# Optimization experiments

Measured on AMD Instinct MI355X. Metric: run time of the kernel, lower is better.

Reference implementation:

```python
import jax, jax.numpy as jnp
import numpy as np

DILATIONS = (1, 3, 5)
NUM_HEADS = 2


def _conv(x, w, b, dil=1, pad=0):
    # x: [B,C,H,W], w: [O,I,kh,kw] (OIHW), 'same'-style padding = dilation for k=3
    y = jax.lax.conv_general_dilated(
        x, w, window_strides=(1, 1), padding=[(pad, pad), (pad, pad)],
        rhs_dilation=(dil, dil), dimension_numbers=('NCHW', 'OIHW', 'NCHW'))
    return y + b[None, :, None, None]


def setup_inputs() -> dict:
    key = jax.random.key(0)
    ks = jax.random.split(key, 4)
    B, Cin, H, W = 4, 256, 64, 64
    Cout = 256
    x = jax.random.normal(ks[0], (B, Cin, H, W), dtype=jnp.float32)
    # kaiming-uniform-like init scale
    q_w = jax.random.uniform(ks[1], (Cout, Cin, 3, 3), dtype=jnp.float32,
                             minval=-1.0, maxval=1.0) * np.sqrt(6.0 / (Cin * 9))
    k_w = jax.random.uniform(ks[2], (Cout, Cin, 1, 1), dtype=jnp.float32,
                             minval=-1.0, maxval=1.0) * np.sqrt(6.0 / Cin)
    v_w = jax.random.uniform(ks[3], (Cout, Cin, 1, 1), dtype=jnp.float32,
                             minval=-1.0, maxval=1.0) * np.sqrt(6.0 / Cin)
    q_b = jnp.zeros((Cout,), jnp.float32)
    k_b = jnp.zeros((Cout,), jnp.float32)
    v_b = jnp.zeros((Cout,), jnp.float32)
    return {"x": x, "q_w": q_w, "q_b": q_b, "k_w": k_w, "k_b": k_b,
            "v_w": v_w, "v_b": v_b}


def reference(x, q_w, q_b, k_w, k_b, v_w, v_b):
    B, C, H, W = x.shape
    Cout = q_w.shape[0]
    hd = Cout // NUM_HEADS  # head_dim
    # ds_conv2d: sum of SiLU(dilated conv) over dilations 1,3,5 (padding=dilation)
    q = sum(jax.nn.silu(_conv(x, q_w, q_b, dil=d, pad=d)) for d in DILATIONS)
    k = _conv(x, k_w, k_b)
    v = _conv(x, v_w, v_b)
    N = H * W
    # [B, heads, head_dim, N]
    q = q.reshape(B, NUM_HEADS, hd, N)
    k = k.reshape(B, NUM_HEADS, hd, N)
    v = v.reshape(B, NUM_HEADS, hd, N)
    # energy[b,h,n,m] = sum_d q[b,h,d,n] * k[b,h,d,m]
    energy = jnp.einsum('bhdn,bhdm->bhnm', q, k)
    attn = jax.nn.softmax(energy / jnp.sqrt(jnp.float32(hd)), axis=-1)
    # out[b,h,n,d] = sum_m attn[b,h,n,m] * v[b,h,d,m]; then back to [B,C,H,W]
    out = jnp.einsum('bhnm,bhdm->bhdn', attn, v)
    return out.reshape(B, Cout, H, W)
```

## Files before the change

kernel.cpp:

```cpp
#include <hip/hip_runtime.h>
#include <cstdint>

typedef __attribute__((ext_vector_type(8))) _Float16 f16x8;
typedef __attribute__((ext_vector_type(4))) float f32x4;

#define DEV static __device__ __forceinline__

DEV void gld_lds16(void* lds_base, const void* gsrc) {
  __builtin_amdgcn_global_load_lds(
      (const __attribute__((address_space(1))) unsigned int*)gsrc,
      (__attribute__((address_space(3))) unsigned int*)lds_base,
      16, 0, 0);
}
DEV unsigned short f2h(float f) {
  _Float16 h = (_Float16)f;
  return __builtin_bit_cast(unsigned short, h);
}
DEV float h2f(unsigned short u) {
  _Float16 h = __builtin_bit_cast(_Float16, u);
  return (float)h;
}
DEV unsigned pk2h(float a, float b) {
  auto h2 = __builtin_amdgcn_cvt_pkrtz(a, b);
  return __builtin_bit_cast(unsigned, h2);
}
DEV float v_exp2(float x) { float r; asm("v_exp_f32 %0, %1" : "=v"(r) : "v"(x)); return r; }
DEV float v_rcp(float x) { float r; asm("v_rcp_f32 %0, %1" : "=v"(r) : "v"(x)); return r; }


__global__ __launch_bounds__(256) void k_prep_x(const float* __restrict__ x, char* __restrict__ xpad) {
  __shared__ float xs[32 * 257];
  int h = blockIdx.x, b = blockIdx.y, t = threadIdx.x;
  const float* xb = x + (size_t)b * 1048576 + h * 64;
  for (int half = 0; half < 2; half++) {
    int w0 = half * 32;
    for (int kk = 0; kk < 32; kk++) {
      int flat = kk * 256 + t;
      int ci = flat >> 5, w = flat & 31;
      xs[w * 257 + ci] = xb[ci * 4096 + w0 + w];
    }
    __syncthreads();
    for (int g = 0; g < 4; g++) {
      int w = g * 8 + (t >> 5);
      int cg = t & 31;
      float v0 = xs[w * 257 + cg * 8 + 0], v1 = xs[w * 257 + cg * 8 + 1];
      float v2 = xs[w * 257 + cg * 8 + 2], v3 = xs[w * 257 + cg * 8 + 3];
      float v4 = xs[w * 257 + cg * 8 + 4], v5 = xs[w * 257 + cg * 8 + 5];
      float v6 = xs[w * 257 + cg * 8 + 6], v7 = xs[w * 257 + cg * 8 + 7];
      uint4 pk;
      pk.x = pk2h(v0, v1);
      pk.y = pk2h(v2, v3);
      pk.z = pk2h(v4, v5);
      pk.w = pk2h(v6, v7);
      *(uint4*)(xpad + ((size_t)((b * 74 + h + 5) * 74) + w0 + w + 5) * 512 + cg * 16) = pk;
    }
    __syncthreads();
  }
}

__global__ __launch_bounds__(256) void k_prep_w(
    const float* __restrict__ qw, const float* __restrict__ kw, const float* __restrict__ vw,
    unsigned short* __restrict__ Wq, unsigned short* __restrict__ Wk, unsigned short* __restrict__ Wv) {
  int gid = blockIdx.x * 256 + threadIdx.x;
  const float* q9 = qw + (size_t)gid * 9;
#pragma unroll
  for (int tp = 0; tp < 9; tp++) Wq[tp * 65536 + gid] = f2h(q9[tp]);
  Wk[gid] = f2h(kw[gid]);
  Wv[gid] = f2h(vw[gid]);
}

__global__ __launch_bounds__(256, 2) void k_conv_kv(
    const char* __restrict__ xpad, const unsigned short* __restrict__ Wk,
    const unsigned short* __restrict__ Wv, const float* __restrict__ kb,
    const float* __restrict__ vb, unsigned short* __restrict__ K, unsigned short* __restrict__ V) {
  __shared__ char sm[32768];
  char* Xs = sm;
  char* Ws = sm + 16384;
  int t = threadIdx.x, lane = t & 63, wid = t >> 6, q4 = lane >> 4, l15 = lane & 15;
  int px0 = blockIdx.x * 128;
  int b = px0 >> 12, nn = px0 & 4095;
  int h = blockIdx.y;
  int mode = blockIdx.z;
  int co0 = h * 128;
  const char* Wsrc = (const char*)(mode ? Wv : Wk);
  int wm = wid & 1, wn = wid >> 1;
  f32x4 acc[4][4] = {};
  for (int c = 0; c < 4; c++) {
    __syncthreads();
    for (int ch = wid * 1024; ch < 16384; ch += 4096) {
      int o = ch + lane * 16;
      int r = o >> 7;
      int n = nn + r, hh = n >> 6, ww2 = n & 63;
      int col = (o & 127) ^ ((r & 7) << 4);
      gld_lds16(Xs + ch, xpad + ((size_t)((b * 74 + hh + 5) * 74) + ww2 + 5) * 512 + c * 128 + col);
    }
    for (int ch = wid * 1024; ch < 16384; ch += 4096) {
      int o = ch + lane * 16;
      int r = o >> 7;
      int col = (o & 127) ^ ((r & 7) << 4);
      gld_lds16(Ws + ch, Wsrc + (co0 + r) * 512 + c * 128 + col);
    }
    asm volatile("s_waitcnt vmcnt(0)" ::: "memory");
    __syncthreads();
    int xg = mode ? wn : wm;
    int wg = mode ? wm : wn;
#pragma unroll
    for (int kt = 0; kt < 2; kt++) {
      f16x8 xf[4], wf[4];
#pragma unroll
      for (int i = 0; i < 4; i++) {
        int rx = xg * 64 + i * 16 + l15;
        xf[i] = *(const f16x8*)(Xs + ((rx * 128 + kt * 64 + q4 * 16) ^ ((rx & 7) << 4)));
        int rw = wg * 64 + i * 16 + l15;
        wf[i] = *(const f16x8*)(Ws + ((rw * 128 + kt * 64 + q4 * 16) ^ ((rw & 7) << 4)));
      }
#pragma unroll
      for (int m = 0; m < 4; m++)
#pragma unroll
        for (int n = 0; n < 4; n++)
          acc[m][n] = mode ? __builtin_amdgcn_mfma_f32_16x16x32_f16(wf[m], xf[n], acc[m][n], 0, 0, 0)
                           : __builtin_amdgcn_mfma_f32_16x16x32_f16(xf[m], wf[n], acc[m][n], 0, 0, 0);
    }
  }
  int bh = b * 2 + h;
  if (mode == 0) {
#pragma unroll
    for (int m = 0; m < 4; m++)
#pragma unroll
      for (int n = 0; n < 4; n++) {
        int dd = wn * 64 + n * 16 + l15;
        float bias = kb[co0 + dd];
#pragma unroll
        for (int j = 0; j < 4; j++) {
          int npix = nn + wm * 64 + m * 16 + q4 * 4 + j;
          K[(size_t)(bh * 4096 + npix) * 128 + dd] = f2h(acc[m][n][j] + bias);
        }
      }
  } else {
#pragma unroll
    for (int m = 0; m < 4; m++)
#pragma unroll
      for (int j = 0; j < 4; j++) {
        int cr = wm * 64 + m * 16 + q4 * 4 + j;
        float bias = vb[co0 + cr];
#pragma unroll
        for (int n = 0; n < 4; n++) {
          int pc = nn + wn * 64 + (n >> 1) * 32 + (l15 >> 2) * 8 + (n & 1) * 4 + (l15 & 3);
          V[(size_t)(bh * 128 + cr) * 4096 + pc] = f2h(acc[m][n][j] + bias);
        }
      }
  }
}

__global__ __launch_bounds__(256, 2) void k_conv_q(
    const char* __restrict__ xpad, const unsigned short* __restrict__ Wq,
    const float* __restrict__ qb, unsigned short* __restrict__ Q) {
  extern __shared__ char sm[];
  char* Bs = sm;
  char* As = sm + 49152;
  int t = threadIdx.x, lane = t & 63, wid = t >> 6, q4 = lane >> 4, l15 = lane & 15;
  int fblk = blockIdx.x;
  int g = (fblk & 7) * 64 + (fblk >> 3);
  int h = g & 63, b = (g >> 6) & 3, ch2 = g >> 8;
  int co0 = ch2 * 128;
  int wm = wid & 1, wn = wid >> 1;
  const int dil[3] = {1, 3, 5};
  f32x4 accd[3][2][4] = {};
  for (int kh = 0; kh < 3; kh++) {
    for (int c = 0; c < 4; c++) {
      __syncthreads();
      const char* wq_base = (const char*)Wq + kh * 3 * 131072 + co0 * 512 + c * 128;
      for (int ch = wid * 1024; ch < 49152; ch += 4096) {
        int o = ch + lane * 16;
        int kw = o >> 14;
        int r = (o >> 7) & 127;
        int col = (o & 127) ^ ((r & 7) << 4);
        gld_lds16(Bs + ch, wq_base + kw * 131072 + r * 512 + col);
      }
      int nst = (kh == 1) ? 1 : 3;
      for (int di = 0; di < nst; di++) {
        int pr = h + (kh - 1) * dil[di] + 5;
        const char* gsrc = xpad + (size_t)((b * 74 + pr) * 74) * 512 + c * 128;
        char* Ad = As + di * 10240;
        for (int ch = wid * 1024; ch < 9472; ch += 4096) {
          int o = ch + lane * 16;
          if (o < 9472) {
            int r = o >> 7;
            int col = (o & 127) ^ ((r & 7) << 4);
            gld_lds16(Ad + ch, gsrc + r * 512 + col);
          }
        }
      }
      asm volatile("s_waitcnt vmcnt(0)" ::: "memory");
      __syncthreads();
#pragma unroll
      for (int kw = 0; kw < 3; kw++) {
        f16x8 bf[4][2];
#pragma unroll
        for (int n = 0; n < 4; n++)
#pragma unroll
          for (int kt = 0; kt < 2; kt++) {
            int rc = wn * 64 + n * 16 + l15;
            bf[n][kt] = *(const f16x8*)(Bs + kw * 16384 + ((rc * 128 + kt * 64 + q4 * 16) ^ ((rc & 7) << 4)));
          }
#pragma unroll
        for (int di = 0; di < 3; di++) {
          int d = dil[di];
          const char* Ad = As + (kh == 1 ? 0 : di) * 10240;
          int dw = (kw - 1) * d + 5;
          f16x8 af[2][2];
#pragma unroll
          for (int m = 0; m < 2; m++)
#pragma unroll
            for (int kt = 0; kt < 2; kt++) {
              int wp = wm * 32 + m * 16 + l15 + dw;
              af[m][kt] = *(const f16x8*)(Ad + ((wp * 128 + kt * 64 + q4 * 16) ^ ((wp & 7) << 4)));
            }
#pragma unroll
          for (int m = 0; m < 2; m++)
#pragma unroll
            for (int n = 0; n < 4; n++)
#pragma unroll
              for (int kt = 0; kt < 2; kt++)
                accd[di][m][n] = __builtin_amdgcn_mfma_f32_16x16x32_f16(af[m][kt], bf[n][kt], accd[di][m][n], 0, 0, 0);
        }
      }
    }
  }
  const float LOG2E = 1.4426950408889634f;
  const float QSCALE = 0.12751879523176862f;
#pragma unroll
  for (int n = 0; n < 4; n++) {
    float bias = qb[co0 + wn * 64 + n * 16 + l15];
#pragma unroll
    for (int m = 0; m < 2; m++)
#pragma unroll
      for (int j = 0; j < 4; j++) {
        float s = 0.f;
#pragma unroll
        for (int di = 0; di < 3; di++) {
          float v = accd[di][m][n][j] + bias;
          s += v * v_rcp(1.0f + v_exp2(-v * LOG2E));
        }
        int px = wm * 32 + m * 16 + q4 * 4 + j;
        int dd = wn * 64 + n * 16 + l15;
        int npix = h * 64 + px;
        Q[((size_t)(b * 2 + ch2) * 4096 + npix) * 128 + dd] = f2h(s * QSCALE);
      }
  }
}

__global__ __launch_bounds__(256, 2) void k_attn(
    const unsigned short* __restrict__ Q, const unsigned short* __restrict__ K,
    const unsigned short* __restrict__ V, float* __restrict__ out,
    unsigned short* __restrict__ o1buf, float* __restrict__ mlbuf) {
  __shared__ char sm[65536];
  char* K0 = sm;
  char* K1 = sm + 16384;
  char* V0 = sm + 32768;
  char* V1 = sm + 49152;
  int t = threadIdx.x, lane = t & 63, wid = t >> 6, q4 = lane >> 4, l15 = lane & 15;
  int fblk = blockIdx.x;
  int g = (fblk & 7) * 64 + (fblk >> 3);
  int nb = g & 31, bh = (g >> 5) & 7, half = g >> 8;
  int b = bh >> 1, hh = bh & 1;
  int n0 = nb * 128;
  const char* Qg = (const char*)(Q + ((size_t)bh * 4096 + n0) * 128);
  const char* Kg = (const char*)(K + (size_t)bh * 4096 * 128) + half * 524288;
  const char* Vg = (const char*)(V + (size_t)bh * 128 * 4096) + half * 4096;
  f16x8 qf[2][4];
#pragma unroll
  for (int nt = 0; nt < 2; nt++)
#pragma unroll
    for (int kt = 0; kt < 4; kt++) {
      int rn = wid * 32 + nt * 16 + l15;
      qf[nt][kt] = *(const f16x8*)(Qg + (size_t)rn * 256 + kt * 64 + q4 * 16);
    }
  for (int ch = wid * 1024; ch < 16384; ch += 4096) {
    int o = ch + lane * 16;
    gld_lds16(K0 + ch, Kg + (o ^ (((o >> 8) & 15) << 4)));
  }
  for (int ch = wid * 1024; ch < 16384; ch += 4096) {
    int o = ch + lane * 16;
    int dd = o >> 7;
    int col = (o & 127) ^ ((dd & 7) << 4);
    gld_lds16(V0 + ch, Vg + dd * 8192 + col);
  }
  asm volatile("s_waitcnt vmcnt(0)" ::: "memory");
  __syncthreads();
  f32x4 Ofr[8][2] = {};
  float mrun[2] = {-3e38f, -3e38f};
  float lrun[2] = {0.f, 0.f};
  for (int it = 0; it < 32; it++) {
    char* Kc = (it & 1) ? K1 : K0;
    char* Vc = (it & 1) ? V1 : V0;
    if (it < 31) {
      char* Kn = (it & 1) ? K0 : K1;
      char* Vn = (it & 1) ? V0 : V1;
      const char* kg = Kg + (size_t)(it + 1) * 16384;
      for (int ch = wid * 1024; ch < 16384; ch += 4096) {
        int o = ch + lane * 16;
        gld_lds16(Kn + ch, kg + (o ^ (((o >> 8) & 15) << 4)));
      }
      const char* vg = Vg + (it + 1) * 128;
      for (int ch = wid * 1024; ch < 16384; ch += 4096) {
        int o = ch + lane * 16;
        int dd = o >> 7;
        int col = (o & 127) ^ ((dd & 7) << 4);
        gld_lds16(Vn + ch, vg + dd * 8192 + col);
      }
    }
    f32x4 sT[4][2] = {};
#pragma unroll
    for (int kt = 0; kt < 4; kt++) {
      f16x8 kf[4];
#pragma unroll
      for (int mt = 0; mt < 4; mt++) {
        int rm = mt * 16 + l15;
        kf[mt] = *(const f16x8*)(Kc + ((rm * 256 + kt * 64 + q4 * 16) ^ ((rm & 15) << 4)));
      }
      __builtin_amdgcn_s_setprio(1);
#pragma unroll
      for (int mt = 0; mt < 4; mt++)
#pragma unroll
        for (int nt = 0; nt < 2; nt++)
          sT[mt][nt] = __builtin_amdgcn_mfma_f32_16x16x32_f16(kf[mt], qf[nt][kt], sT[mt][nt], 0, 0, 0);
      __builtin_amdgcn_s_setprio(0);
    }
    unsigned U[2][4][2];
#pragma unroll
    for (int nt = 0; nt < 2; nt++) {
      float mx = sT[0][nt][0];
#pragma unroll
      for (int mt = 0; mt < 4; mt++)
#pragma unroll
        for (int j = 0; j < 4; j++) mx = fmaxf(mx, sT[mt][nt][j]);
      mx = fmaxf(mx, __shfl_xor(mx, 16));
      mx = fmaxf(mx, __shfl_xor(mx, 32));
      float mn = mrun[nt];
      if (!__all(mx - mn <= 8.f)) {
        mn = fmaxf(mrun[nt], mx);
        float al = v_exp2(mrun[nt] - mn);
        mrun[nt] = mn;
        lrun[nt] *= al;
#pragma unroll
        for (int dt = 0; dt < 8; dt++) Ofr[dt][nt] *= al;
      }
      float rs = 0.f;
#pragma unroll
      for (int mt = 0; mt < 4; mt++) {
        float p0 = v_exp2(sT[mt][nt][0] - mn);
        float p1 = v_exp2(sT[mt][nt][1] - mn);
        float p2 = v_exp2(sT[mt][nt][2] - mn);
        float p3 = v_exp2(sT[mt][nt][3] - mn);
        rs += (p0 + p1) + (p2 + p3);
        U[nt][mt][0] = pk2h(p0, p1);
        U[nt][mt][1] = pk2h(p2, p3);
      }
      rs += __shfl_xor(rs, 16);
      rs += __shfl_xor(rs, 32);
      lrun[nt] += rs;
    }
#pragma unroll
    for (int kt = 0; kt < 2; kt++) {
      f16x8 pf[2];
#pragma unroll
      for (int nt = 0; nt < 2; nt++) {
        uint4 fr;
        fr.x = U[nt][2 * kt][0];
        fr.y = U[nt][2 * kt][1];
        fr.z = U[nt][2 * kt + 1][0];
        fr.w = U[nt][2 * kt + 1][1];
        pf[nt] = __builtin_bit_cast(f16x8, fr);
      }
      f16x8 vf[8];
#pragma unroll
      for (int dt = 0; dt < 8; dt++) {
        int rd = dt * 16 + l15;
        vf[dt] = *(const f16x8*)(Vc + ((rd * 128 + kt * 64 + q4 * 16) ^ ((rd & 7) << 4)));
      }
      __builtin_amdgcn_s_setprio(1);
#pragma unroll
      for (int dt = 0; dt < 8; dt++)
#pragma unroll
        for (int nt = 0; nt < 2; nt++)
          Ofr[dt][nt] = __builtin_amdgcn_mfma_f32_16x16x32_f16(vf[dt], pf[nt], Ofr[dt][nt], 0, 0, 0);
      __builtin_amdgcn_s_setprio(0);
    }
    __syncthreads();
  }
  if (q4 == 0) {
#pragma unroll
    for (int nt = 0; nt < 2; nt++) {
      int n = n0 + wid * 32 + nt * 16 + l15;
      float2 ml;
      ml.x = mrun[nt];
      ml.y = lrun[nt];
      *(float2*)(mlbuf + ((size_t)(half * 8 + bh) * 4096 + n) * 2) = ml;
    }
  }
  if (half == 0) {
    float* og = out + (size_t)(b * 256 + hh * 128) * 4096 + n0 + wid * 32;
#pragma unroll
    for (int dt = 0; dt < 8; dt++)
#pragma unroll
      for (int nt = 0; nt < 2; nt++)
#pragma unroll
        for (int j = 0; j < 4; j++) {
          int dd = dt * 16 + q4 * 4 + j;
          og[(size_t)dd * 4096 + nt * 16 + l15] = Ofr[dt][nt][j];
        }
  } else {
    float li[2] = {v_rcp(lrun[0]), v_rcp(lrun[1])};
    unsigned short* og = o1buf + (size_t)bh * 128 * 4096 + n0 + wid * 32;
#pragma unroll
    for (int dt = 0; dt < 8; dt++)
#pragma unroll
      for (int nt = 0; nt < 2; nt++)
#pragma unroll
        for (int j = 0; j < 4; j++) {
          int dd = dt * 16 + q4 * 4 + j;
          og[(size_t)dd * 4096 + nt * 16 + l15] = f2h(Ofr[dt][nt][j] * li[nt]);
        }
  }
}

__global__ __launch_bounds__(256) void k_combine(
    float* __restrict__ out, const unsigned short* __restrict__ o1,
    const float* __restrict__ ml) {
  int tid = blockIdx.x * 256 + threadIdx.x;
  int n = tid & 4095, dg = (tid >> 12) & 7, bh = tid >> 15;
  float2 ml0 = *(const float2*)(ml + ((size_t)bh * 4096 + n) * 2);
  float2 ml1 = *(const float2*)(ml + ((size_t)(8 + bh) * 4096 + n) * 2);
  float ms = fmaxf(ml0.x, ml1.x);
  float a0 = v_exp2(ml0.x - ms);
  float w1 = ml1.y * v_exp2(ml1.x - ms);
  float inv = 1.f / (ml0.y * a0 + w1);
  size_t ob = ((size_t)((bh >> 1) * 256 + (bh & 1) * 128 + dg * 16)) * 4096 + n;
  size_t o1b = ((size_t)(bh * 128 + dg * 16)) * 4096 + n;
#pragma unroll 4
  for (int j = 0; j < 16; j++) {
    float v0 = out[ob + (size_t)j * 4096];
    float v1 = h2f(o1[o1b + (size_t)j * 4096]);
    out[ob + (size_t)j * 4096] = (v0 * a0 + v1 * w1) * inv;
  }
}

extern "C" void kernel_launch(void* const* d_in, const int* in_sizes, int n_in,
                              void* d_out, int out_size, void* d_ws, size_t ws_size,
                              hipStream_t stream) {
  (void)in_sizes; (void)n_in; (void)out_size;
  const float* x  = (const float*)d_in[0];
  const float* qw = (const float*)d_in[1];
  const float* qb = (const float*)d_in[2];
  const float* kw = (const float*)d_in[3];
  const float* kb = (const float*)d_in[4];
  const float* vw = (const float*)d_in[5];
  const float* vb = (const float*)d_in[6];
  char* ws = (char*)d_ws;
  if (ws_size < 37822464) return;
  char* xpad = ws;
  unsigned short* Wq = (unsigned short*)(ws + 11214848);
  unsigned short* Wk = (unsigned short*)(ws + 12394496);
  unsigned short* Wv = (unsigned short*)(ws + 12525568);
  unsigned short* Qb = (unsigned short*)(ws + 12656640);
  unsigned short* Kb = (unsigned short*)(ws + 21045248);
  unsigned short* Vb = (unsigned short*)(ws + 29433856);
  unsigned short* O1 = (unsigned short*)ws;
  float* ML = (float*)(ws + 11214848);
  hipMemsetAsync(xpad, 0, 11214848, stream);
  k_prep_x<<<dim3(64, 4), dim3(256), 0, stream>>>(x, xpad);
  k_prep_w<<<dim3(256), dim3(256), 0, stream>>>(qw, kw, vw, Wq, Wk, Wv);
  k_conv_kv<<<dim3(128, 2, 2), dim3(256), 0, stream>>>(xpad, Wk, Wv, kb, vb, Kb, Vb);
  k_conv_q<<<dim3(512), dim3(256), 79872, stream>>>(xpad, Wq, qb, Qb);
  k_attn<<<dim3(512), dim3(256), 0, stream>>>(Qb, Kb, Vb, (float*)d_out, O1, ML);
  k_combine<<<dim3(1024), dim3(256), 0, stream>>>((float*)d_out, O1, ML);
}
```

Measured before the change: 179.7 us.

## Restructure dilated Q conv: two rows per block, double-buffered weight staging

The Q convolution kernel now runs 512 threads per block, each block covering two output image rows, so every weight tile loaded into LDS is reused across twice as many pixels and the grid halves. Weight tiles are staged one kw slice at a time into a double buffer, with the next slice prefetched while MFMAs run on the current one. MFMA bursts are also wrapped in s_setprio. Costs include a larger LDS footprint (89.6KB), a barrier after every kw step, and input-row staging that still waits synchronously.

New measurement: 179.2 us. About the same (-0.2%).

```diff
diff --git a/kernel.cpp b/kernel.cpp
--- a/kernel.cpp
+++ b/kernel.cpp
@@ -152,70 +152,95 @@
   }
 }
 
-__global__ __launch_bounds__(256, 2) void k_conv_q(
+__global__ __launch_bounds__(512, 2) void k_conv_q(
     const char* __restrict__ xpad, const unsigned short* __restrict__ Wq,
     const float* __restrict__ qb, unsigned short* __restrict__ Q) {
   extern __shared__ char sm[];
-  char* Bs = sm;
-  char* As = sm + 49152;
+  char* As = sm + 32768;
   int t = threadIdx.x, lane = t & 63, wid = t >> 6, q4 = lane >> 4, l15 = lane & 15;
   int fblk = blockIdx.x;
-  int g = (fblk & 7) * 64 + (fblk >> 3);
-  int h = g & 63, b = (g >> 6) & 3, ch2 = g >> 8;
+  int g = (fblk & 7) * 32 + (fblk >> 3);
+  int h2 = g & 31, b = (g >> 5) & 3, ch2 = g >> 7;
+  int h0 = h2 * 2;
   int co0 = ch2 * 128;
-  int wm = wid & 1, wn = wid >> 1;
+  int wn = wid & 1, wq = wid >> 1;
+  int hr = wq >> 1, wloc = wq & 1;
   const int dil[3] = {1, 3, 5};
+  const char* WqB = (const char*)Wq;
   f32x4 accd[3][2][4] = {};
+
+#define STAGE_B(dstbuf, kh_, c_, kw_)                                             \
+  {                                                                               \
+    const char* src_ = WqB + (size_t)((kh_)*3 + (kw_)) * 131072 + co0 * 512 + (c_)*128; \
+    char* dst_ = (dstbuf);                                                        \
+    for (int ch = wid * 1024; ch < 16384; ch += 8192) {                           \
+      int o = ch + lane * 16;                                                     \
+      int r = o >> 7;                                                             \
+      int col = (o & 127) ^ ((r & 7) << 4);                                       \
+      gld_lds16(dst_ + ch, src_ + r * 512 + col);                                 \
+    }                                                                             \
+  }
+
+#define STAGE_A_ROW(slot_, pr_, c_)                                               \
+  {                                                                               \
+    const char* src_ = xpad + ((size_t)(b * 74 + (pr_)) * 74) * 512 + (c_)*128;   \
+    char* dst_ = As + (slot_)*9472;                                               \
+    for (int ch = wid * 1024; ch < 9472; ch += 8192) {                            \
+      int o = ch + lane * 16;                                                     \
+      if (o < 9472) {                                                             \
+        int r = o >> 7;                                                           \
+        int col = (o & 127) ^ ((r & 7) << 4);                                     \
+        gld_lds16(dst_ + ch, src_ + r * 512 + col);                               \
+      }                                                                           \
+    }                                                                             \
+  }
+
+#define STAGE_A(kh_, c_)                                                          \
+  {                                                                               \
+    if ((kh_) == 1) {                                                             \
+      for (int s = 0; s < 2; s++) STAGE_A_ROW(s, h0 + s + 5, c_);                 \
+    } else {                                                                      \
+      for (int di = 0; di < 3; di++)                                              \
+        for (int s = 0; s < 2; s++)                                               \
+          STAGE_A_ROW(di * 2 + s, h0 + s + ((kh_)-1) * dil[di] + 5, c_);          \
+    }                                                                             \
+  }
+
+  STAGE_A(0, 0);
+  STAGE_B(sm, 0, 0, 0);
+  asm volatile("s_waitcnt vmcnt(0)" ::: "memory");
+  __syncthreads();
+
+  int cur = 0;
   for (int kh = 0; kh < 3; kh++) {
     for (int c = 0; c < 4; c++) {
-      __syncthreads();
-      const char* wq_base = (const char*)Wq + kh * 3 * 131072 + co0 * 512 + c * 128;
-      for (int ch = wid * 1024; ch < 49152; ch += 4096) {
-        int o = ch + lane * 16;
-        int kw = o >> 14;
-        int r = (o >> 7) & 127;
-        int col = (o & 127) ^ ((r & 7) << 4);
-        gld_lds16(Bs + ch, wq_base + kw * 131072 + r * 512 + col);
-      }
-      int nst = (kh == 1) ? 1 : 3;
-      for (int di = 0; di < nst; di++) {
-        int pr = h + (kh - 1) * dil[di] + 5;
-        const char* gsrc = xpad + (size_t)((b * 74 + pr) * 74) * 512 + c * 128;
-        char* Ad = As + di * 10240;
-        for (int ch = wid * 1024; ch < 9472; ch += 4096) {
-          int o = ch + lane * 16;
-          if (o < 9472) {
-            int r = o >> 7;
-            int col = (o & 127) ^ ((r & 7) << 4);
-            gld_lds16(Ad + ch, gsrc + r * 512 + col);
-          }
-        }
-      }
-      asm volatile("s_waitcnt vmcnt(0)" ::: "memory");
-      __syncthreads();
-#pragma unroll
       for (int kw = 0; kw < 3; kw++) {
+        int kwn = kw + 1, cn = c, khn = kh;
+        if (kwn == 3) { kwn = 0; cn = c + 1; if (cn == 4) { cn = 0; khn = kh + 1; } }
+        char* Bnext = cur ? sm : sm + 16384;
+        if (khn < 3) STAGE_B(Bnext, khn, cn, kwn);
+        const char* Bc = cur ? sm + 16384 : sm;
         f16x8 bf[4][2];
 #pragma unroll
         for (int n = 0; n < 4; n++)
 #pragma unroll
           for (int kt = 0; kt < 2; kt++) {
             int rc = wn * 64 + n * 16 + l15;
-            bf[n][kt] = *(const f16x8*)(Bs + kw * 16384 + ((rc * 128 + kt * 64 + q4 * 16) ^ ((rc & 7) << 4)));
+            bf[n][kt] = *(const f16x8*)(Bc + ((rc * 128 + kt * 64 + q4 * 16) ^ ((rc & 7) << 4)));
           }
 #pragma unroll
         for (int di = 0; di < 3; di++) {
-          int d = dil[di];
-          const char* Ad = As + (kh == 1 ? 0 : di) * 10240;
-          int dw = (kw - 1) * d + 5;
+          int dw = (kw - 1) * dil[di] + 5;
+          const char* Ad = As + (kh == 1 ? hr : di * 2 + hr) * 9472;
           f16x8 af[2][2];
 #pragma unroll
           for (int m = 0; m < 2; m++)
 #pragma unroll
             for (int kt = 0; kt < 2; kt++) {
-              int wp = wm * 32 + m * 16 + l15 + dw;
+              int wp = wloc * 32 + m * 16 + l15 + dw;
               af[m][kt] = *(const f16x8*)(Ad + ((wp * 128 + kt * 64 + q4 * 16) ^ ((wp & 7) << 4)));
             }
+          __builtin_amdgcn_s_setprio(1);
 #pragma unroll
           for (int m = 0; m < 2; m++)
 #pragma unroll
@@ -223,10 +248,24 @@
 #pragma unroll
               for (int kt = 0; kt < 2; kt++)
                 accd[di][m][n] = __builtin_amdgcn_mfma_f32_16x16x32_f16(af[m][kt], bf[n][kt], accd[di][m][n], 0, 0, 0);
+          __builtin_amdgcn_s_setprio(0);
         }
-      }
-    }
-  }
+        asm volatile("s_waitcnt vmcnt(0)" ::: "memory");
+        __syncthreads();
+        cur ^= 1;
+      }
+      int cn2 = c + 1, khn2 = kh;
+      if (cn2 == 4) { cn2 = 0; khn2 = kh + 1; }
+      if (khn2 < 3) {
+        STAGE_A(khn2, cn2);
+        asm volatile("s_waitcnt vmcnt(0)" ::: "memory");
+        __syncthreads();
+      }
+    }
+  }
+#undef STAGE_A
+#undef STAGE_A_ROW
+#undef STAGE_B
   const float LOG2E = 1.4426950408889634f;
   const float QSCALE = 0.12751879523176862f;
 #pragma unroll
@@ -242,9 +281,9 @@
           float v = accd[di][m][n][j] + bias;
           s += v * v_rcp(1.0f + v_exp2(-v * LOG2E));
         }
-        int px = wm * 32 + m * 16 + q4 * 4 + j;
+        int w = wloc * 32 + m * 16 + q4 * 4 + j;
+        int npix = (h0 + hr) * 64 + w;
         int dd = wn * 64 + n * 16 + l15;
-        int npix = h * 64 + px;
         Q[((size_t)(b * 2 + ch2) * 4096 + npix) * 128 + dd] = f2h(s * QSCALE);
       }
   }
@@ -472,7 +511,7 @@
   k_prep_x<<<dim3(64, 4), dim3(256), 0, stream>>>(x, xpad);
   k_prep_w<<<dim3(256), dim3(256), 0, stream>>>(qw, kw, vw, Wq, Wk, Wv);
   k_conv_kv<<<dim3(128, 2, 2), dim3(256), 0, stream>>>(xpad, Wk, Wv, kb, vb, Kb, Vb);
-  k_conv_q<<<dim3(512), dim3(256), 79872, stream>>>(xpad, Wq, qb, Qb);
+  k_conv_q<<<dim3(256), dim3(512), 89600, stream>>>(xpad, Wq, qb, Qb);
   k_attn<<<dim3(512), dim3(256), 0, stream>>>(Qb, Kb, Vb, (float*)d_out, O1, ML);
   k_combine<<<dim3(1024), dim3(256), 0, stream>>>((float*)d_out, O1, ML);
 }
```
